# Optimization experiments

Hardware: AMD Instinct MI355X
Metric: run time of the kernel (lower is better)

The kernel has to match this reference:

```python
import jax, jax.numpy as jnp
import numpy as np

N = 100000   # total nodes in batch
E = 1200000  # total edges
D = 64       # dim_features (== hidden_dim)
H = 64       # hidden_dim
T = 32       # dim_targets
L = 3        # num_layers
G = 500      # number of graphs in batch


def setup_inputs() -> dict:
    key = jax.random.key(0)
    ks = jax.random.split(key, 16)
    s = 0.1
    inp = {
        "x": jax.random.normal(ks[0], (N, D), jnp.float32),
        "src": jax.random.randint(ks[1], (E,), 0, N, jnp.int32),
        "dst": jax.random.randint(ks[2], (E,), 0, N, jnp.int32),
        "graph_ids": jnp.sort(jax.random.randint(ks[3], (N,), 0, G, jnp.int32)),
        # GINConv learnable eps (init 0)
        "eps": jnp.zeros((L,), jnp.float32),
        # per-layer conv apply MLP: Linear(D->H), ReLU, Linear(H->H)
        "conv_w1": jax.random.normal(ks[4], (L, D, H), jnp.float32) * s,
        "conv_b1": jnp.zeros((L, H), jnp.float32),
        "conv_w2": jax.random.normal(ks[5], (L, H, H), jnp.float32) * s,
        "conv_b2": jnp.zeros((L, H), jnp.float32),
        # GraphNorm params
        "gn_weight": jnp.ones((L, H), jnp.float32),
        "gn_bias": jnp.zeros((L, H), jnp.float32),
        "gn_scale": jnp.ones((L, H), jnp.float32),
        # per-layer projection MLP: Linear(H->H), ReLU, Linear(H->T)
        "proj_w1": jax.random.normal(ks[6], (L, H, H), jnp.float32) * s,
        "proj_b1": jnp.zeros((L, H), jnp.float32),
        "proj_w2": jax.random.normal(ks[7], (L, H, T), jnp.float32) * s,
        "proj_b2": jnp.zeros((L, T), jnp.float32),
    }
    return inp


def reference(x, src, dst, graph_ids, eps, conv_w1, conv_b1, conv_w2, conv_b2,
              gn_weight, gn_bias, gn_scale, proj_w1, proj_b1, proj_w2, proj_b2):
    gid = graph_ids
    counts = jax.ops.segment_sum(jnp.ones((N,), x.dtype), gid, num_segments=G)
    safe = jnp.maximum(counts, 1.0)[:, None]  # [G,1] nodes per graph

    feat = x
    outs = []
    for l in range(L):
        # GINConv: (1+eps)*h_i + sum over incoming neighbors
        agg = jax.ops.segment_sum(feat[src], dst, num_segments=N)
        h = (1.0 + eps[l]) * feat + agg
        h = jnp.maximum(h @ conv_w1[l] + conv_b1[l], 0.0) @ conv_w2[l] + conv_b2[l]
        # GraphNorm: per-graph mean/std
        mean = jax.ops.segment_sum(h, gid, num_segments=G) / safe
        sub = h - mean[gid] * gn_scale[l]
        var = jax.ops.segment_sum(sub * sub, gid, num_segments=G) / safe
        std = jnp.sqrt(var + 1e-8)
        h = gn_weight[l] * sub / std[gid] + gn_bias[l]
        feat = jnp.maximum(h, 0.0)
        # projection MLP + per-graph mean pooling
        z = jnp.maximum(feat @ proj_w1[l] + proj_b1[l], 0.0) @ proj_w2[l] + proj_b2[l]
        outs.append(jax.ops.segment_sum(z, gid, num_segments=G) / safe)
    return jnp.concatenate(outs, axis=-1)  # [G, L*T]
```

## Files before the change

### kernel.cpp

```cpp
#include <hip/hip_runtime.h>
#include <math.h>

#define N_NODES 100000
#define N_EDGES 1200000
#define DIM 64
#define TDIM 32
#define NLAYERS 3
#define NGRAPH 500
#define NP (N_NODES + 1)

#define BUCKW 512
#define NBUCK ((N_NODES + BUCKW - 1) / BUCKW)
#define ECHUNK ((N_EDGES + 255) / 256)
#define MLPBL ((N_NODES + 63) / 64)

typedef unsigned short bfu;
typedef __attribute__((ext_vector_type(8))) short short8;
typedef __attribute__((ext_vector_type(4))) float v4f;

__device__ __forceinline__ float bf2f(bfu u) {
    union { unsigned int i; float f; } v; v.i = ((unsigned int)u) << 16; return v.f;
}
__device__ __forceinline__ float bflo(unsigned int d) {
    union { unsigned int i; float f; } v; v.i = d << 16; return v.f;
}
__device__ __forceinline__ float bfhi(unsigned int d) {
    union { unsigned int i; float f; } v; v.i = d & 0xFFFF0000u; return v.f;
}
__device__ __forceinline__ bfu f2bf(float f) {
    union { float f; unsigned int i; } v; v.f = f;
    unsigned int r = v.i + 0x7FFFu + ((v.i >> 16) & 1u);
    return (bfu)(r >> 16);
}

__global__ __launch_bounds__(256) void k_setup(const float* __restrict__ x, bfu* __restrict__ xb,
                                               const int* __restrict__ gid, int* __restrict__ gstart,
                                               float* __restrict__ inv_safe, float* __restrict__ ncnt,
                                               const float* __restrict__ w1, const float* __restrict__ w2,
                                               const float* __restrict__ q1, const float* __restrict__ q2,
                                               bfu* __restrict__ w1t, bfu* __restrict__ w2t,
                                               bfu* __restrict__ q1t, bfu* __restrict__ q2t,
                                               const int* __restrict__ dst, int* __restrict__ bcnt) {
    int b = blockIdx.x, t = threadIdx.x;
    if (b < 6250) {
        int base = (b * 256 + t) * 4;
        float4 v = *(const float4*)&x[base];
        ushort4 o;
        o.x = f2bf(v.x); o.y = f2bf(v.y); o.z = f2bf(v.z); o.w = f2bf(v.w);
        *(ushort4*)&xb[base] = o;
    } else if (b == 6250) {
        for (int tt = t; tt <= NGRAPH; tt += 256) {
            int lo = 0, hi = N_NODES;
            while (lo < hi) {
                int mid = (lo + hi) >> 1;
                if (gid[mid] < tt) lo = mid + 1; else hi = mid;
            }
            gstart[tt] = lo;
        }
        __syncthreads();
        for (int tt = t; tt < NGRAPH; tt += 256) {
            int c = gstart[tt + 1] - gstart[tt];
            inv_safe[tt] = 1.0f / (float)(c > 1 ? c : 1);
            ncnt[tt] = (float)c;
        }
    } else if (b < 6299) {
        int i = (b - 6251) * 256 + t;
        int l = i >> 12, k = (i >> 6) & 63, n = i & 63;
        int o = (l << 12) | (n << 6) | k;
        w1t[o] = f2bf(w1[i]);
        w2t[o] = f2bf(w2[i]);
        q1t[o] = f2bf(q1[i]);
        if (i < NLAYERS * 2048) {
            int l2 = i >> 11, rem = i & 2047, k2 = rem >> 5, n2 = rem & 31;
            q2t[l2 * 2048 + n2 * 64 + k2] = f2bf(q2[i]);
        }
    } else {
        __shared__ int h[NBUCK];
        for (int i = t; i < NBUCK; i += 256) h[i] = 0;
        __syncthreads();
        int e0 = (b - 6299) * ECHUNK;
        int e1 = e0 + ECHUNK; if (e1 > N_EDGES) e1 = N_EDGES;
        for (int e = e0 + t; e < e1; e += 256) atomicAdd(&h[dst[e] >> 9], 1);
        __syncthreads();
        for (int i = t; i < NBUCK; i += 256) if (h[i]) atomicAdd(&bcnt[i], h[i]);
    }
}

__global__ __launch_bounds__(256) void k_bscan(const int* __restrict__ bcnt,
                                               int* __restrict__ bbase, int* __restrict__ bcursor,
                                               const int* __restrict__ gstart,
                                               const float* __restrict__ pb2all, float* __restrict__ out) {
    __shared__ int s[256];
    int t = threadIdx.x;
    s[t] = (t < NBUCK) ? bcnt[t] : 0;
    __syncthreads();
    for (int off = 1; off < 256; off <<= 1) {
        int v = (t >= off) ? s[t - off] : 0;
        __syncthreads();
        s[t] += v;
        __syncthreads();
    }
    int ex = t ? s[t - 1] : 0;
    if (t < NBUCK) { bbase[t] = ex; bcursor[t] = ex; }
    if (t == 0) bbase[NBUCK] = N_EDGES;
    for (int g = t; g < NGRAPH; g += 256) {
        int nn = gstart[g + 1] - gstart[g];
        for (int r = 0; r < NLAYERS * TDIM; r++)
            out[g * (NLAYERS * TDIM) + r] = (nn > 0) ? pb2all[r] : 0.f;
    }
}

__global__ __launch_bounds__(256) void k_bscatter(const int* __restrict__ src, const int* __restrict__ dst,
                                                  int* __restrict__ bcursor, int2* __restrict__ ebuf) {
    __shared__ int cnt[NBUCK];
    __shared__ int base[NBUCK];
    int t = threadIdx.x;
    for (int i = t; i < NBUCK; i += 256) cnt[i] = 0;
    __syncthreads();
    int e0 = blockIdx.x * ECHUNK;
    int e1 = e0 + ECHUNK; if (e1 > N_EDGES) e1 = N_EDGES;
    for (int e = e0 + t; e < e1; e += 256) atomicAdd(&cnt[dst[e] >> 9], 1);
    __syncthreads();
    for (int i = t; i < NBUCK; i += 256) base[i] = cnt[i] ? atomicAdd(&bcursor[i], cnt[i]) : 0;
    __syncthreads();
    for (int i = t; i < NBUCK; i += 256) cnt[i] = 0;
    __syncthreads();
    for (int e = e0 + t; e < e1; e += 256) {
        int d = dst[e];
        int b = d >> 9;
        int r = atomicAdd(&cnt[b], 1);
        ebuf[base[b] + r] = make_int2(src[e], d);
    }
}

__global__ __launch_bounds__(256) void k_bcsr(const int2* __restrict__ ebuf, const int* __restrict__ bbase,
                                              int* __restrict__ offs, int* __restrict__ csr) {
    __shared__ int ldeg[BUCKW];
    __shared__ int lscan[BUCKW];
    __shared__ int lcur[BUCKW];
    int t = threadIdx.x;
    int b = blockIdx.x;
    int nbase = b << 9;
    int ebeg = bbase[b], eend = bbase[b + 1];
    ldeg[t] = 0; ldeg[t + 256] = 0;
    __syncthreads();
    for (int e = ebeg + t; e < eend; e += 256) atomicAdd(&ldeg[ebuf[e].y - nbase], 1);
    __syncthreads();
    lscan[t] = ldeg[t]; lscan[t + 256] = ldeg[t + 256];
    __syncthreads();
    for (int off = 1; off < BUCKW; off <<= 1) {
        int i0 = t, i1 = t + 256;
        int v0 = (i0 >= off) ? lscan[i0 - off] : 0;
        int v1 = (i1 >= off) ? lscan[i1 - off] : 0;
        __syncthreads();
        lscan[i0] += v0; lscan[i1] += v1;
        __syncthreads();
    }
    int ex0 = lscan[t] - ldeg[t];
    int ex1 = lscan[t + 256] - ldeg[t + 256];
    lcur[t] = ex0; lcur[t + 256] = ex1;
    int n0 = nbase + t, n1 = nbase + t + 256;
    if (n0 < N_NODES) offs[n0] = ebeg + ex0;
    if (n1 < N_NODES) offs[n1] = ebeg + ex1;
    if (b == 0 && t == 0) offs[N_NODES] = N_EDGES;
    __syncthreads();
    for (int e = ebeg + t; e < eend; e += 256) {
        int2 p = ebuf[e];
        int slot = atomicAdd(&lcur[p.y - nbase], 1);
        csr[ebeg + slot] = p.x;
    }
}

__device__ __forceinline__ void accum8(float* acc, uint4 d) {
    acc[0] += bflo(d.x); acc[1] += bfhi(d.x);
    acc[2] += bflo(d.y); acc[3] += bfhi(d.y);
    acc[4] += bflo(d.z); acc[5] += bfhi(d.z);
    acc[6] += bflo(d.w); acc[7] += bfhi(d.w);
}

__global__ __launch_bounds__(256) void k_agg(const bfu* __restrict__ feat, const int* __restrict__ offs,
                                             const int* __restrict__ csr, const float* __restrict__ eps,
                                             int l, bfu* __restrict__ hin) {
    int w = threadIdx.x >> 6;
    int lane = threadIdx.x & 63;
    int node = blockIdx.x * 4 + w;
    if (node >= N_NODES) return;
    int eidx = lane >> 3;
    int chunk = lane & 7;
    int coff = chunk * 8;
    int e0 = offs[node], e1 = offs[node + 1];
    int eL = e1 - 1;
    float acc[8] = {0.f, 0.f, 0.f, 0.f, 0.f, 0.f, 0.f, 0.f};

    for (int e = e0; e < e1; e += 16) {
        int ea = e + eidx;
        int ca = (ea < eL) ? ea : eL;
        int sa = csr[ca];
        uint4 da = *(const uint4*)&feat[sa * DIM + coff];
        bool two = (e + 8) < e1;
        if (two) {
            int ebi = e + 8 + eidx;
            int cb = (ebi < eL) ? ebi : eL;
            int sb = csr[cb];
            uint4 db = *(const uint4*)&feat[sb * DIM + coff];
            if (ea >= e1) da = make_uint4(0u, 0u, 0u, 0u);
            if (ebi >= e1) db = make_uint4(0u, 0u, 0u, 0u);
            accum8(acc, da);
            accum8(acc, db);
        } else {
            if (ea >= e1) da = make_uint4(0u, 0u, 0u, 0u);
            accum8(acc, da);
        }
    }

#pragma unroll
    for (int j = 0; j < 8; j++) {
        float v = acc[j];
        v += __shfl_xor(v, 8, 64);
        v += __shfl_xor(v, 16, 64);
        v += __shfl_xor(v, 32, 64);
        acc[j] = v;
    }

    float ep = 1.0f + eps[l];
    uint4 s = *(const uint4*)&feat[node * DIM + coff];
    float r0 = ep * bflo(s.x) + acc[0], r1 = ep * bfhi(s.x) + acc[1];
    float r2 = ep * bflo(s.y) + acc[2], r3 = ep * bfhi(s.y) + acc[3];
    float r4 = ep * bflo(s.z) + acc[4], r5 = ep * bfhi(s.z) + acc[5];
    float r6 = ep * bflo(s.w) + acc[6], r7 = ep * bfhi(s.w) + acc[7];
    if (eidx == 0) {
        uint4 o;
        o.x = ((unsigned int)f2bf(r1) << 16) | f2bf(r0);
        o.y = ((unsigned int)f2bf(r3) << 16) | f2bf(r2);
        o.z = ((unsigned int)f2bf(r5) << 16) | f2bf(r4);
        o.w = ((unsigned int)f2bf(r7) << 16) | f2bf(r6);
        *(uint4*)&hin[node * DIM + coff] = o;
    }
}

__global__ __launch_bounds__(256) void k_mlp(const bfu* __restrict__ hin,
                                             const bfu* __restrict__ w1t, const float* __restrict__ b1,
                                             const bfu* __restrict__ w2t, const float* __restrict__ b2,
                                             const int* __restrict__ gid, bfu* __restrict__ hout,
                                             float* __restrict__ gsum, float* __restrict__ gsq) {
    __shared__ bfu ldsT[4][16 * 80];
    __shared__ int sG[4][16];
    int t = threadIdx.x;
    int w = t >> 6, lane = t & 63, m = lane & 15, q = lane >> 4;
    int nbase = blockIdx.x * 64 + w * 16;
    int row = nbase + m;
    bool valid = row < N_NODES;
    if (lane < 16) sG[w][lane] = (nbase + lane < N_NODES) ? gid[nbase + lane] : -1;

    short8 a0 = {0, 0, 0, 0, 0, 0, 0, 0}, a1 = a0;
    if (valid) {
        a0 = *(const short8*)&hin[row * 64 + q * 8];
        a1 = *(const short8*)&hin[row * 64 + 32 + q * 8];
    }
    short8 bf1[4][2], bf2[4][2];
#pragma unroll
    for (int ct = 0; ct < 4; ct++)
#pragma unroll
        for (int kk = 0; kk < 2; kk++) {
            bf1[ct][kk] = *(const short8*)&w1t[(ct * 16 + m) * 64 + kk * 32 + q * 8];
            bf2[ct][kk] = *(const short8*)&w2t[(ct * 16 + m) * 64 + kk * 32 + q * 8];
        }

    bfu* my = ldsT[w];
#pragma unroll
    for (int ct = 0; ct < 4; ct++) {
        float bv = b1[ct * 16 + m];
        v4f acc = {bv, bv, bv, bv};
        acc = __builtin_amdgcn_mfma_f32_16x16x32_bf16(a0, bf1[ct][0], acc, 0, 0, 0);
        acc = __builtin_amdgcn_mfma_f32_16x16x32_bf16(a1, bf1[ct][1], acc, 0, 0, 0);
#pragma unroll
        for (int r = 0; r < 4; r++)
            my[(q * 4 + r) * 80 + ct * 16 + m] = f2bf(fmaxf(acc[r], 0.f));
    }
    short8 a20 = *(short8*)&my[m * 80 + q * 8];
    short8 a21 = *(short8*)&my[m * 80 + 32 + q * 8];
#pragma unroll
    for (int ct = 0; ct < 4; ct++) {
        float bv = b2[ct * 16 + m];
        v4f acc = {bv, bv, bv, bv};
        acc = __builtin_amdgcn_mfma_f32_16x16x32_bf16(a20, bf2[ct][0], acc, 0, 0, 0);
        acc = __builtin_amdgcn_mfma_f32_16x16x32_bf16(a21, bf2[ct][1], acc, 0, 0, 0);
#pragma unroll
        for (int r = 0; r < 4; r++)
            my[(q * 4 + r) * 80 + ct * 16 + m] = f2bf(acc[r]);
    }
#pragma unroll
    for (int i = 0; i < 2; i++) {
        int idx = i * 64 + lane;
        int r = idx >> 3, ch = (idx & 7) * 8;
        int grow = nbase + r;
        uint4 v = *(uint4*)&my[r * 80 + ch];
        if (grow < N_NODES) *(uint4*)&hout[grow * 64 + ch] = v;
    }
    float s_acc = 0.f, q_acc = 0.f;
    int cur = sG[w][0];
    for (int r = 0; r < 16; r++) {
        int g2 = sG[w][r];
        if (g2 != cur) {
            if (cur >= 0) {
                atomicAdd(&gsum[cur * 64 + lane], s_acc);
                atomicAdd(&gsq[cur * 64 + lane], q_acc);
            }
            cur = g2; s_acc = 0.f; q_acc = 0.f;
        }
        if (g2 >= 0) {
            float v = bf2f(my[r * 80 + lane]);
            s_acc += v; q_acc += v * v;
        }
    }
    if (cur >= 0) {
        atomicAdd(&gsum[cur * 64 + lane], s_acc);
        atomicAdd(&gsq[cur * 64 + lane], q_acc);
    }
}

__global__ __launch_bounds__(256) void k_apply_proj(const bfu* __restrict__ h,
                                                    const int* __restrict__ gid,
                                                    const float* __restrict__ gsum,
                                                    const float* __restrict__ gsq,
                                                    const float* __restrict__ inv_safe,
                                                    const float* __restrict__ ncnt,
                                                    const float* __restrict__ gnw, const float* __restrict__ gnb,
                                                    const float* __restrict__ gns,
                                                    const bfu* __restrict__ p1t, const float* __restrict__ pb1,
                                                    const bfu* __restrict__ p2t,
                                                    bfu* __restrict__ feat, float* __restrict__ out, int l) {
    __shared__ bfu ldsT[4][16 * 80];
    __shared__ float sZ[64 * 33];
    __shared__ int sGid[64];
    int t = threadIdx.x;
    int w = t >> 6, lane = t & 63, m = lane & 15, q = lane >> 4;
    int row0 = blockIdx.x * 64;
    int row = row0 + w * 16 + m;
    bool valid = row < N_NODES;
    if (t < 64) sGid[t] = (row0 + t < N_NODES) ? gid[row0 + t] : -1;

    union Pack { short8 v; bfu u[8]; uint4 qv; };
    Pack a0, a1;
    a0.qv = make_uint4(0u, 0u, 0u, 0u);
    a1.qv = make_uint4(0u, 0u, 0u, 0u);
    if (valid) {
        int g = gid[row];
        float inv = inv_safe[g];
        float nnf = ncnt[g];
#pragma unroll
        for (int kk = 0; kk < 2; kk++) {
            int ch = kk * 32 + q * 8;
            uint4 hv = *(const uint4*)&h[row * 64 + ch];
            float4 Sa = *(const float4*)&gsum[g * 64 + ch];
            float4 Sb = *(const float4*)&gsum[g * 64 + ch + 4];
            float4 Qa = *(const float4*)&gsq[g * 64 + ch];
            float4 Qb = *(const float4*)&gsq[g * 64 + ch + 4];
            float4 nsa = *(const float4*)&gns[ch];
            float4 nsb = *(const float4*)&gns[ch + 4];
            float4 nwa = *(const float4*)&gnw[ch];
            float4 nwb = *(const float4*)&gnw[ch + 4];
            float4 gba = *(const float4*)&gnb[ch];
            float4 gbb = *(const float4*)&gnb[ch + 4];
            float hval[8] = {bflo(hv.x), bfhi(hv.x), bflo(hv.y), bfhi(hv.y),
                             bflo(hv.z), bfhi(hv.z), bflo(hv.w), bfhi(hv.w)};
            float Sv[8] = {Sa.x, Sa.y, Sa.z, Sa.w, Sb.x, Sb.y, Sb.z, Sb.w};
            float Qv[8] = {Qa.x, Qa.y, Qa.z, Qa.w, Qb.x, Qb.y, Qb.z, Qb.w};
            float nsv[8] = {nsa.x, nsa.y, nsa.z, nsa.w, nsb.x, nsb.y, nsb.z, nsb.w};
            float nwv[8] = {nwa.x, nwa.y, nwa.z, nwa.w, nwb.x, nwb.y, nwb.z, nwb.w};
            float gbv[8] = {gba.x, gba.y, gba.z, gba.w, gbb.x, gbb.y, gbb.z, gbb.w};
            Pack& a = kk ? a1 : a0;
#pragma unroll
            for (int j = 0; j < 8; j++) {
                float ms = Sv[j] * inv * nsv[j];
                float var = (Qv[j] - 2.f * ms * Sv[j] + nnf * ms * ms) * inv;
                float coef = nwv[j] * rsqrtf(var + 1e-8f);
                a.u[j] = f2bf(fmaxf(coef * (hval[j] - ms) + gbv[j], 0.f));
            }
            *(uint4*)&feat[row * 64 + ch] = a.qv;
        }
    }

    short8 bf1[4][2], bf2[2][2];
#pragma unroll
    for (int ct = 0; ct < 4; ct++)
#pragma unroll
        for (int kk = 0; kk < 2; kk++)
            bf1[ct][kk] = *(const short8*)&p1t[(ct * 16 + m) * 64 + kk * 32 + q * 8];
#pragma unroll
    for (int ct = 0; ct < 2; ct++)
#pragma unroll
        for (int kk = 0; kk < 2; kk++)
            bf2[ct][kk] = *(const short8*)&p2t[(ct * 16 + m) * 64 + kk * 32 + q * 8];

    bfu* tl = ldsT[w];
#pragma unroll
    for (int ct = 0; ct < 4; ct++) {
        float bv = pb1[ct * 16 + m];
        v4f acc = {bv, bv, bv, bv};
        acc = __builtin_amdgcn_mfma_f32_16x16x32_bf16(a0.v, bf1[ct][0], acc, 0, 0, 0);
        acc = __builtin_amdgcn_mfma_f32_16x16x32_bf16(a1.v, bf1[ct][1], acc, 0, 0, 0);
#pragma unroll
        for (int r = 0; r < 4; r++)
            tl[(q * 4 + r) * 80 + ct * 16 + m] = f2bf(fmaxf(acc[r], 0.f));
    }
    short8 a20 = *(short8*)&tl[m * 80 + q * 8];
    short8 a21 = *(short8*)&tl[m * 80 + 32 + q * 8];
#pragma unroll
    for (int ct = 0; ct < 2; ct++) {
        v4f acc = {0.f, 0.f, 0.f, 0.f};
        acc = __builtin_amdgcn_mfma_f32_16x16x32_bf16(a20, bf2[ct][0], acc, 0, 0, 0);
        acc = __builtin_amdgcn_mfma_f32_16x16x32_bf16(a21, bf2[ct][1], acc, 0, 0, 0);
#pragma unroll
        for (int r = 0; r < 4; r++)
            sZ[(w * 16 + q * 4 + r) * 33 + ct * 16 + m] = acc[r];
    }
    __syncthreads();

    if (t < 32) {
        int cur = sGid[0];
        float a = 0.f;
        for (int r = 0; r < 64; r++) {
            int g2 = sGid[r];
            if (g2 != cur) {
                if (cur >= 0) atomicAdd(&out[cur * (NLAYERS * TDIM) + l * TDIM + t], a * inv_safe[cur]);
                cur = g2;
                a = 0.f;
            }
            if (g2 >= 0) a += sZ[r * 33 + t];
        }
        if (cur >= 0) atomicAdd(&out[cur * (NLAYERS * TDIM) + l * TDIM + t], a * inv_safe[cur]);
    }
}


extern "C" void kernel_launch(void* const* d_in, const int* in_sizes, int n_in,
                              void* d_out, int out_size, void* d_ws, size_t ws_size,
                              hipStream_t stream) {
    const float* x        = (const float*)d_in[0];
    const int*   src      = (const int*)d_in[1];
    const int*   dst      = (const int*)d_in[2];
    const int*   gid      = (const int*)d_in[3];
    const float* eps      = (const float*)d_in[4];
    const float* conv_w1  = (const float*)d_in[5];
    const float* conv_b1  = (const float*)d_in[6];
    const float* conv_w2  = (const float*)d_in[7];
    const float* conv_b2  = (const float*)d_in[8];
    const float* gn_w     = (const float*)d_in[9];
    const float* gn_b     = (const float*)d_in[10];
    const float* gn_s     = (const float*)d_in[11];
    const float* proj_w1  = (const float*)d_in[12];
    const float* proj_b1  = (const float*)d_in[13];
    const float* proj_w2  = (const float*)d_in[14];
    const float* proj_b2  = (const float*)d_in[15];
    float* out = (float*)d_out;

    char* ws = (char*)d_ws;
    size_t off = 0;
    auto alloc = [&](size_t bytes) { char* p = ws + off; off += (bytes + 255) & ~(size_t)255; return p; };
    int*   offs     = (int*)alloc(NP * sizeof(int));
    int*   gstart   = (int*)alloc((NGRAPH + 1) * sizeof(int));
    float* inv_safe = (float*)alloc(NGRAPH * sizeof(float));
    float* ncnt     = (float*)alloc(NGRAPH * sizeof(float));
    int*   bcnt     = (int*)alloc(NBUCK * sizeof(int));
    float* gsumA    = (float*)alloc((size_t)NLAYERS * 2 * NGRAPH * 64 * sizeof(float));
    size_t zbytes   = (size_t)((char*)(gsumA + (size_t)NLAYERS * 2 * NGRAPH * 64) - (char*)bcnt);
    int*   bbase    = (int*)alloc((NBUCK + 1) * sizeof(int));
    int*   bcursor  = (int*)alloc(NBUCK * sizeof(int));
    int*   csr      = (int*)alloc(N_EDGES * sizeof(int));
    bfu*   featbf   = (bfu*)alloc((size_t)N_NODES * DIM * sizeof(bfu));
    bfu*   hinbf    = (bfu*)alloc((size_t)N_NODES * DIM * sizeof(bfu));
    bfu*   hbufbf   = (bfu*)alloc((size_t)N_NODES * DIM * sizeof(bfu));
    bfu*   w1t      = (bfu*)alloc((size_t)NLAYERS * 4096 * sizeof(bfu));
    bfu*   w2t      = (bfu*)alloc((size_t)NLAYERS * 4096 * sizeof(bfu));
    bfu*   p1t      = (bfu*)alloc((size_t)NLAYERS * 4096 * sizeof(bfu));
    bfu*   p2t      = (bfu*)alloc((size_t)NLAYERS * 2048 * sizeof(bfu));
    int2*  ebuf     = (int2*)alloc((size_t)N_EDGES * sizeof(int2));

    hipMemsetAsync(bcnt, 0, zbytes, stream);
    k_setup<<<6555, 256, 0, stream>>>(x, featbf, gid, gstart, inv_safe, ncnt,
                                      conv_w1, conv_w2, proj_w1, proj_w2, w1t, w2t, p1t, p2t,
                                      dst, bcnt);
    k_bscan<<<1, 256, 0, stream>>>(bcnt, bbase, bcursor, gstart, proj_b2, out);
    k_bscatter<<<256, 256, 0, stream>>>(src, dst, bcursor, ebuf);
    k_bcsr<<<NBUCK, 256, 0, stream>>>(ebuf, bbase, offs, csr);

    int aggbl = (N_NODES + 3) / 4;
    for (int l = 0; l < NLAYERS; l++) {
        float* gsum_l = gsumA + (size_t)l * 2 * NGRAPH * 64;
        float* gsq_l  = gsum_l + NGRAPH * 64;
        k_agg<<<aggbl, 256, 0, stream>>>(featbf, offs, csr, eps, l, hinbf);
        k_mlp<<<MLPBL, 256, 0, stream>>>(hinbf, w1t + l * 4096, conv_b1 + l * 64,
                                         w2t + l * 4096, conv_b2 + l * 64,
                                         gid, hbufbf, gsum_l, gsq_l);
        k_apply_proj<<<MLPBL, 256, 0, stream>>>(hbufbf, gid, gsum_l, gsq_l, inv_safe, ncnt,
                                                gn_w + l * 64, gn_b + l * 64, gn_s + l * 64,
                                                p1t + l * 4096, proj_b1 + l * 64,
                                                p2t + l * 2048, featbf, out, l);
    }
}
```

Before: 443.0 us.

## Remap aggregation to 16 threads per node with sequential edge loop

The CSR gather-sum kernel changes from one 64-lane wavefront per node (8 edges in parallel, 8-wide bf16 chunks, shuffle reduction) to 16 threads per node, each handling 4 features and walking all edges two at a time. This removes the cross-lane shuffle reduction, the idle lanes on low-degree nodes and the masked-out stores, and packs 4 nodes per wavefront. In exchange each thread issues narrower 8-byte loads and runs a longer serial loop, and nodes of different degree in the same wavefront can diverge.

```diff
diff --git a/kernel.cpp b/kernel.cpp
--- a/kernel.cpp
+++ b/kernel.cpp
@@ -171,71 +171,42 @@
     }
 }
 
-__device__ __forceinline__ void accum8(float* acc, uint4 d) {
-    acc[0] += bflo(d.x); acc[1] += bfhi(d.x);
-    acc[2] += bflo(d.y); acc[3] += bfhi(d.y);
-    acc[4] += bflo(d.z); acc[5] += bfhi(d.z);
-    acc[6] += bflo(d.w); acc[7] += bfhi(d.w);
-}
-
 __global__ __launch_bounds__(256) void k_agg(const bfu* __restrict__ feat, const int* __restrict__ offs,
                                              const int* __restrict__ csr, const float* __restrict__ eps,
                                              int l, bfu* __restrict__ hin) {
-    int w = threadIdx.x >> 6;
-    int lane = threadIdx.x & 63;
-    int node = blockIdx.x * 4 + w;
+    int t = threadIdx.x;
+    int sub = t & 15;
+    int node = blockIdx.x * 16 + (t >> 4);
     if (node >= N_NODES) return;
-    int eidx = lane >> 3;
-    int chunk = lane & 7;
-    int coff = chunk * 8;
+    int coff = sub * 4;
     int e0 = offs[node], e1 = offs[node + 1];
     int eL = e1 - 1;
-    float acc[8] = {0.f, 0.f, 0.f, 0.f, 0.f, 0.f, 0.f, 0.f};
-
-    for (int e = e0; e < e1; e += 16) {
-        int ea = e + eidx;
-        int ca = (ea < eL) ? ea : eL;
-        int sa = csr[ca];
-        uint4 da = *(const uint4*)&feat[sa * DIM + coff];
-        bool two = (e + 8) < e1;
-        if (two) {
-            int ebi = e + 8 + eidx;
-            int cb = (ebi < eL) ? ebi : eL;
-            int sb = csr[cb];
-            uint4 db = *(const uint4*)&feat[sb * DIM + coff];
-            if (ea >= e1) da = make_uint4(0u, 0u, 0u, 0u);
-            if (ebi >= e1) db = make_uint4(0u, 0u, 0u, 0u);
-            accum8(acc, da);
-            accum8(acc, db);
-        } else {
-            if (ea >= e1) da = make_uint4(0u, 0u, 0u, 0u);
-            accum8(acc, da);
-        }
-    }
-
-#pragma unroll
-    for (int j = 0; j < 8; j++) {
-        float v = acc[j];
-        v += __shfl_xor(v, 8, 64);
-        v += __shfl_xor(v, 16, 64);
-        v += __shfl_xor(v, 32, 64);
-        acc[j] = v;
+    float acc0 = 0.f, acc1 = 0.f, acc2 = 0.f, acc3 = 0.f;
+
+    for (int e = e0; e < e1; e += 2) {
+        int eb = e + 1;
+        int cb = (eb < e1) ? eb : eL;
+        int sa = csr[e];
+        int sb = csr[cb];
+        uint2 da = *(const uint2*)&feat[sa * DIM + coff];
+        uint2 db = *(const uint2*)&feat[sb * DIM + coff];
+        if (eb >= e1) { db.x = 0u; db.y = 0u; }
+        acc0 += bflo(da.x); acc1 += bfhi(da.x);
+        acc2 += bflo(da.y); acc3 += bfhi(da.y);
+        acc0 += bflo(db.x); acc1 += bfhi(db.x);
+        acc2 += bflo(db.y); acc3 += bfhi(db.y);
     }
 
     float ep = 1.0f + eps[l];
-    uint4 s = *(const uint4*)&feat[node * DIM + coff];
-    float r0 = ep * bflo(s.x) + acc[0], r1 = ep * bfhi(s.x) + acc[1];
-    float r2 = ep * bflo(s.y) + acc[2], r3 = ep * bfhi(s.y) + acc[3];
-    float r4 = ep * bflo(s.z) + acc[4], r5 = ep * bfhi(s.z) + acc[5];
-    float r6 = ep * bflo(s.w) + acc[6], r7 = ep * bfhi(s.w) + acc[7];
-    if (eidx == 0) {
-        uint4 o;
-        o.x = ((unsigned int)f2bf(r1) << 16) | f2bf(r0);
-        o.y = ((unsigned int)f2bf(r3) << 16) | f2bf(r2);
-        o.z = ((unsigned int)f2bf(r5) << 16) | f2bf(r4);
-        o.w = ((unsigned int)f2bf(r7) << 16) | f2bf(r6);
-        *(uint4*)&hin[node * DIM + coff] = o;
-    }
+    uint2 s = *(const uint2*)&feat[node * DIM + coff];
+    float r0 = ep * bflo(s.x) + acc0;
+    float r1 = ep * bfhi(s.x) + acc1;
+    float r2 = ep * bflo(s.y) + acc2;
+    float r3 = ep * bfhi(s.y) + acc3;
+    uint2 o;
+    o.x = ((unsigned int)f2bf(r1) << 16) | f2bf(r0);
+    o.y = ((unsigned int)f2bf(r3) << 16) | f2bf(r2);
+    *(uint2*)&hin[node * DIM + coff] = o;
 }
 
 __global__ __launch_bounds__(256) void k_mlp(const bfu* __restrict__ hin,
@@ -485,7 +456,7 @@
     k_bscatter<<<256, 256, 0, stream>>>(src, dst, bcursor, ebuf);
     k_bcsr<<<NBUCK, 256, 0, stream>>>(ebuf, bbase, offs, csr);
 
-    int aggbl = (N_NODES + 3) / 4;
+    int aggbl = (N_NODES + 15) / 16;
     for (int l = 0; l < NLAYERS; l++) {
         float* gsum_l = gsumA + (size_t)l * 2 * NGRAPH * 64;
         float* gsq_l  = gsum_l + NGRAPH * 64;
```

Result: faster. 422.0 us (-4.7%).
